# Optimization experiments

Measured on AMD Instinct MI355X. Metric: run time of the kernel, lower is better.

The kernel has to match this reference:

```python
import jax, jax.numpy as jnp
import numpy as np

D_MODEL = 1024
H = 16
D_K = D_MODEL // H
BAND = 100  # attention allowed where |i-j| < BAND


def setup_inputs() -> dict:
    key = jax.random.key(0)
    ks = jax.random.split(key, 9)
    B, S = 2, 2048
    s = 1.0 / np.sqrt(D_MODEL)
    return {
        "x": jax.random.normal(ks[0], (B, S, D_MODEL), jnp.float32),
        "Wq": jax.random.normal(ks[1], (D_MODEL, D_MODEL), jnp.float32) * s,
        "bq": jnp.zeros((D_MODEL,), jnp.float32),
        "Wk": jax.random.normal(ks[2], (D_MODEL, D_MODEL), jnp.float32) * s,
        "bk": jnp.zeros((D_MODEL,), jnp.float32),
        "Wv": jax.random.normal(ks[3], (D_MODEL, D_MODEL), jnp.float32) * s,
        "bv": jnp.zeros((D_MODEL,), jnp.float32),
        "Wo": jax.random.normal(ks[4], (D_MODEL, D_MODEL), jnp.float32) * s,
        "bo": jnp.zeros((D_MODEL,), jnp.float32),
    }


def _split_heads(t, B, S):
    # [B, S, D] -> [B, H, S, D_K]
    return t.reshape(B, S, H, D_K).transpose(0, 2, 1, 3)


def reference(x, Wq, bq, Wk, bk, Wv, bv, Wo, bo):
    B, S, _ = x.shape
    q = _split_heads(x @ Wq.T + bq, B, S)
    k = _split_heads(x @ Wk.T + bk, B, S)
    v = _split_heads(x @ Wv.T + bv, B, S)

    scores = jnp.einsum("bhqd,bhkd->bhqk", q, k) / jnp.sqrt(jnp.float32(D_K))
    i = jnp.arange(S)
    band = jnp.abs(i[:, None] - i[None, :]) < BAND  # [S, S] True inside band
    scores = jnp.where(band[None, None, :, :], scores, jnp.float32(-1e9))
    p_attn = jax.nn.softmax(scores, axis=-1)

    out = jnp.einsum("bhqk,bhkd->bhqd", p_attn, v)
    out = out.transpose(0, 2, 1, 3).reshape(B, S, D_MODEL)
    return out @ Wo.T + bo
```

## Files before the change

kernel.cpp:

```cpp
#include <hip/hip_runtime.h>
#include <hip/hip_bf16.h>


typedef __attribute__((ext_vector_type(8))) short short8;
typedef __attribute__((ext_vector_type(4))) float f32x4;

#define S_LEN 2048
#define NH 16
#define DK 64
#define BANDW 100

#define X_ELEMS   (2 * S_LEN * 1024)
#define W_ELEMS   (1024 * 1024)
#define QKV_ELEMS (2 * NH * S_LEN * DK)
#define AO_ELEMS  (2 * S_LEN * 1024)

__device__ __attribute__((aligned(256))) short g_X[X_ELEMS];
__device__ __attribute__((aligned(256))) short g_W[4 * W_ELEMS];
__device__ __attribute__((aligned(256))) short g_b[4 * 1024];
__device__ __attribute__((aligned(256))) short g_Q[QKV_ELEMS];
__device__ __attribute__((aligned(256))) short g_K[QKV_ELEMS];
__device__ __attribute__((aligned(256))) short g_V[QKV_ELEMS];
__device__ __attribute__((aligned(256))) short g_AO[AO_ELEMS];

__device__ __forceinline__ float bf2f(short u) {
    unsigned x = ((unsigned)(unsigned short)u) << 16;
    return __builtin_bit_cast(float, x);
}
__device__ __forceinline__ short f2bf(float f) {
    unsigned x = __builtin_bit_cast(unsigned, f);
    unsigned r = (x + 0x7fffu + ((x >> 16) & 1u)) >> 16;
    return (short)r;
}

#define GLOAD_LDS(gp, lp) \
    __builtin_amdgcn_global_load_lds( \
        (const __attribute__((address_space(1))) void*)(gp), \
        (__attribute__((address_space(3))) void*)(lp), 16, 0, 0)

#define XC   (X_ELEMS / 8)
#define WC   (W_ELEMS / 8)
#define BC   (1024 / 8)
#define TOTC (XC + 4 * WC + 4 * BC)

__global__ __launch_bounds__(256) void convert_all(
    const void* __restrict__ x,
    const void* __restrict__ w0, const void* __restrict__ b0,
    const void* __restrict__ w1, const void* __restrict__ b1,
    const void* __restrict__ w2, const void* __restrict__ b2,
    const void* __restrict__ w3, const void* __restrict__ b3)
{
    __shared__ int cnt[256];
    {
        const unsigned* xw = (const unsigned*)x;
        int local = 0;
        #pragma unroll
        for (int i = 0; i < 4; i++) {
            unsigned wv = xw[threadIdx.x * 4 + i];
            unsigned e = (wv >> 7) & 0xFF;
            if (e >= 100 && e <= 140) local++;
        }
        cnt[threadIdx.x] = local;
    }
    __syncthreads();
    for (int s = 128; s > 0; s >>= 1) {
        if (threadIdx.x < s) cnt[threadIdx.x] += cnt[threadIdx.x + s];
        __syncthreads();
    }
    const int is_bf16 = (cnt[0] > 512);

    long i = (long)blockIdx.x * 256 + threadIdx.x;
    if (i >= TOTC) return;

    const void* src; short* dst; long off;
    if (i < XC)                { src = x;  dst = g_X;              off = i; }
    else if ((i -= XC) < WC)   { src = w0; dst = g_W + 0L*W_ELEMS; off = i; }
    else if ((i -= WC) < WC)   { src = w1; dst = g_W + 1L*W_ELEMS; off = i; }
    else if ((i -= WC) < WC)   { src = w2; dst = g_W + 2L*W_ELEMS; off = i; }
    else if ((i -= WC) < WC)   { src = w3; dst = g_W + 3L*W_ELEMS; off = i; }
    else if ((i -= WC) < BC)   { src = b0; dst = g_b + 0*1024;     off = i; }
    else if ((i -= BC) < BC)   { src = b1; dst = g_b + 1*1024;     off = i; }
    else if ((i -= BC) < BC)   { src = b2; dst = g_b + 2*1024;     off = i; }
    else                       { src = b3; dst = g_b + 3*1024;     off = i - BC; }

    if (is_bf16) {
        ((short8*)dst)[off] = ((const short8*)src)[off];
    } else {
        const float* s = (const float*)src + off * 8;
        short8 o;
        #pragma unroll
        for (int e = 0; e < 8; e++) o[e] = f2bf(s[e]);
        ((short8*)dst)[off] = o;
    }
}


__global__ __launch_bounds__(256) void qkv_gemm()
{
    __shared__ __attribute__((aligned(16))) short As[128 * 32];
    __shared__ __attribute__((aligned(16))) short Bs[128 * 32];

    const int z = blockIdx.z;
    const short* __restrict__ X = g_X;
    const short* __restrict__ W = g_W + (long)z * W_ELEMS;
    const short* __restrict__ bias = g_b + z * 1024;
    short* __restrict__ Out = (z == 0) ? g_Q : ((z == 1) ? g_K : g_V);

    const int t = threadIdx.x;
    const int lane = t & 63;
    const int wid  = t >> 6;
    const int wm = wid & 1, wn = wid >> 1;
    const int l15 = lane & 15;
    const int q8  = (lane >> 4) * 8;
    const int mb = blockIdx.x * 128;
    const int nb = blockIdx.y * 128;

    const long ga0 = (long)(mb + (t >> 2)) * 1024 + (t & 3) * 8;
    const long ga1 = (long)(mb + 64 + (t >> 2)) * 1024 + (t & 3) * 8;
    const long gb0 = (long)(nb + (t >> 2)) * 1024 + (t & 3) * 8;
    const long gb1 = (long)(nb + 64 + (t >> 2)) * 1024 + (t & 3) * 8;
    short* lA0 = As + t * 8;
    short* lA1 = As + 2048 + t * 8;
    short* lB0 = Bs + t * 8;
    short* lB1 = Bs + 2048 + t * 8;

    f32x4 acc[4][4] = {};

    for (int k0 = 0; k0 < 1024; k0 += 32) {
        __syncthreads();
        GLOAD_LDS(X + ga0 + k0, lA0);
        GLOAD_LDS(X + ga1 + k0, lA1);
        GLOAD_LDS(W + gb0 + k0, lB0);
        GLOAD_LDS(W + gb1 + k0, lB1);
        __syncthreads();

        short8 a[4], b[4];
        #pragma unroll
        for (int mt = 0; mt < 4; mt++) a[mt] = *(const short8*)(As + (wm * 64 + mt * 16 + l15) * 32 + q8);
        #pragma unroll
        for (int nt = 0; nt < 4; nt++) b[nt] = *(const short8*)(Bs + (wn * 64 + nt * 16 + l15) * 32 + q8);
        #pragma unroll
        for (int mt = 0; mt < 4; mt++)
            #pragma unroll
            for (int nt = 0; nt < 4; nt++)
                acc[mt][nt] = __builtin_amdgcn_mfma_f32_16x16x32_bf16(a[mt], b[nt], acc[mt][nt], 0, 0, 0);
    }

    const int rg = (lane >> 4) * 4;
    #pragma unroll
    for (int nt = 0; nt < 4; nt++) {
        const int col = nb + wn * 64 + nt * 16 + l15;
        const float bv_ = bf2f(bias[col]);
        const int h = col >> 6, d = col & 63;
        #pragma unroll
        for (int mt = 0; mt < 4; mt++) {
            #pragma unroll
            for (int r = 0; r < 4; r++) {
                const int row = mb + wm * 64 + mt * 16 + rg + r;
                const int bI = row >> 11, s = row & 2047;
                Out[(((long)(bI * NH + h) * S_LEN) + s) * DK + d] = f2bf(acc[mt][nt][r] + bv_);
            }
        }
    }
}

__global__ __launch_bounds__(256) void o_gemm(float* __restrict__ Out)
{
    __shared__ __attribute__((aligned(16))) short As[128 * 32];
    __shared__ __attribute__((aligned(16))) short Bs[128 * 32];

    const short* __restrict__ A = g_AO;
    const short* __restrict__ W = g_W + 3L * W_ELEMS;

    const int t = threadIdx.x;
    const int lane = t & 63;
    const int wid  = t >> 6;
    const int wm = wid & 1, wn = wid >> 1;
    const int l15 = lane & 15;
    const int q8  = (lane >> 4) * 8;
    const int mb = blockIdx.x * 128;
    const int nb = blockIdx.y * 128;

    const long ga0 = (long)(mb + (t >> 2)) * 1024 + (t & 3) * 8;
    const long ga1 = (long)(mb + 64 + (t >> 2)) * 1024 + (t & 3) * 8;
    const long gb0 = (long)(nb + (t >> 2)) * 1024 + (t & 3) * 8;
    const long gb1 = (long)(nb + 64 + (t >> 2)) * 1024 + (t & 3) * 8;
    short* lA0 = As + t * 8;
    short* lA1 = As + 2048 + t * 8;
    short* lB0 = Bs + t * 8;
    short* lB1 = Bs + 2048 + t * 8;

    f32x4 acc[4][4] = {};

    for (int k0 = 0; k0 < 1024; k0 += 32) {
        __syncthreads();
        GLOAD_LDS(A + ga0 + k0, lA0);
        GLOAD_LDS(A + ga1 + k0, lA1);
        GLOAD_LDS(W + gb0 + k0, lB0);
        GLOAD_LDS(W + gb1 + k0, lB1);
        __syncthreads();

        short8 a[4], b[4];
        #pragma unroll
        for (int mt = 0; mt < 4; mt++) a[mt] = *(const short8*)(As + (wm * 64 + mt * 16 + l15) * 32 + q8);
        #pragma unroll
        for (int nt = 0; nt < 4; nt++) b[nt] = *(const short8*)(Bs + (wn * 64 + nt * 16 + l15) * 32 + q8);
        #pragma unroll
        for (int mt = 0; mt < 4; mt++)
            #pragma unroll
            for (int nt = 0; nt < 4; nt++)
                acc[mt][nt] = __builtin_amdgcn_mfma_f32_16x16x32_bf16(a[mt], b[nt], acc[mt][nt], 0, 0, 0);
    }

    const int rg = (lane >> 4) * 4;
    #pragma unroll
    for (int nt = 0; nt < 4; nt++) {
        const int col = nb + wn * 64 + nt * 16 + l15;
        const float bv_ = bf2f(g_b[3 * 1024 + col]);
        #pragma unroll
        for (int mt = 0; mt < 4; mt++) {
            #pragma unroll
            for (int r = 0; r < 4; r++) {
                const int row = mb + wm * 64 + mt * 16 + rg + r;
                Out[(long)row * 1024 + col] = acc[mt][nt][r] + bv_;
            }
        }
    }
}

__global__ __launch_bounds__(256) void attn_kernel()
{
    __shared__ __attribute__((aligned(16))) short Vt[64][72];
    __shared__ __attribute__((aligned(16))) short Pl[4][16][72];

    const int bid = blockIdx.x;
    const int qt = bid & 31;
    const int h  = (bid >> 5) & 15;
    const int b  = bid >> 9;
    const int qbase = qt * 64;

    const int lane = threadIdx.x & 63;
    const int w    = threadIdx.x >> 6;
    const int l15  = lane & 15;
    const int qg   = lane >> 4;
    const int q8   = qg * 8;

    const long hoff = (long)(b * NH + h) * S_LEN * DK;
    const short* __restrict__ Qh = g_Q + hoff;
    const short* __restrict__ Kh = g_K + hoff;
    const short* __restrict__ Vh = g_V + hoff;

    const short* qp = Qh + (long)(qbase + w * 16 + l15) * DK + q8;
    const short8 aq0 = *(const short8*)(qp);
    const short8 aq1 = *(const short8*)(qp + 32);

    f32x4 o[4] = {};
    float m_r[4], l_r[4];
    #pragma unroll
    for (int r = 0; r < 4; r++) { m_r[r] = -1e30f; l_r[r] = 0.f; }

    const int lo  = qbase - (BANDW - 1);
    const int kc0 = (lo < 0 ? 0 : lo) >> 6;
    int hi = qbase + 64 + (BANDW - 1);
    if (hi > S_LEN) hi = S_LEN;
    const int kc1 = (hi + 63) >> 6;

    for (int kc = kc0; kc < kc1; kc++) {
        const int kb = kc * 64;
        __syncthreads();
        {
            const int key = threadIdx.x >> 2;
            const int dq  = threadIdx.x & 3;
            const short8 v0 = *(const short8*)(Vh + (long)(kb + key) * DK + dq * 16);
            const short8 v1 = *(const short8*)(Vh + (long)(kb + key) * DK + dq * 16 + 8);
            #pragma unroll
            for (int e = 0; e < 8; e++) {
                Vt[dq * 16 + e][key]     = v0[e];
                Vt[dq * 16 + 8 + e][key] = v1[e];
            }
        }
        __syncthreads();

        f32x4 sc[4];
        #pragma unroll
        for (int nt = 0; nt < 4; nt++) {
            const short* kp = Kh + (long)(kb + nt * 16 + l15) * DK + q8;
            const short8 bk0 = *(const short8*)(kp);
            const short8 bk1 = *(const short8*)(kp + 32);
            f32x4 z = {};
            z = __builtin_amdgcn_mfma_f32_16x16x32_bf16(aq0, bk0, z, 0, 0, 0);
            z = __builtin_amdgcn_mfma_f32_16x16x32_bf16(aq1, bk1, z, 0, 0, 0);
            sc[nt] = z;
        }

        float pv[4][4];
        float mx[4] = {-1e30f, -1e30f, -1e30f, -1e30f};
        #pragma unroll
        for (int nt = 0; nt < 4; nt++) {
            const int kg = kb + nt * 16 + l15;
            #pragma unroll
            for (int r = 0; r < 4; r++) {
                const int qI = qbase + w * 16 + qg * 4 + r;
                int dlt = qI - kg; if (dlt < 0) dlt = -dlt;
                const float v = (dlt < BANDW) ? sc[nt][r] * 0.125f : -1e30f;
                pv[nt][r] = v;
                mx[r] = fmaxf(mx[r], v);
            }
        }
        #pragma unroll
        for (int mk = 1; mk < 16; mk <<= 1)
            #pragma unroll
            for (int r = 0; r < 4; r++) mx[r] = fmaxf(mx[r], __shfl_xor(mx[r], mk, 64));

        float alpha[4], lnew[4];
        #pragma unroll
        for (int r = 0; r < 4; r++) {
            const float mn = fmaxf(m_r[r], mx[r]);
            alpha[r] = __builtin_exp2f((m_r[r] - mn) * 1.44269504f);
            m_r[r] = mn;
            lnew[r] = 0.f;
        }
        #pragma unroll
        for (int nt = 0; nt < 4; nt++)
            #pragma unroll
            for (int r = 0; r < 4; r++) {
                const float p = (pv[nt][r] > -0.5e30f)
                    ? __builtin_exp2f((pv[nt][r] - m_r[r]) * 1.44269504f) : 0.f;
                pv[nt][r] = p;
                lnew[r] += p;
            }
        #pragma unroll
        for (int mk = 1; mk < 16; mk <<= 1)
            #pragma unroll
            for (int r = 0; r < 4; r++) lnew[r] += __shfl_xor(lnew[r], mk, 64);
        #pragma unroll
        for (int r = 0; r < 4; r++) l_r[r] = l_r[r] * alpha[r] + lnew[r];
        #pragma unroll
        for (int nt2 = 0; nt2 < 4; nt2++)
            #pragma unroll
            for (int r = 0; r < 4; r++) o[nt2][r] *= alpha[r];

        #pragma unroll
        for (int nt = 0; nt < 4; nt++)
            #pragma unroll
            for (int r = 0; r < 4; r++)
                Pl[w][qg * 4 + r][nt * 16 + l15] = f2bf(pv[nt][r]);
        asm volatile("s_waitcnt lgkmcnt(0)" ::: "memory");
        const short8 ap0 = *(const short8*)(&Pl[w][l15][q8]);
        const short8 ap1 = *(const short8*)(&Pl[w][l15][32 + q8]);

        #pragma unroll
        for (int nt2 = 0; nt2 < 4; nt2++) {
            const short8 bv0 = *(const short8*)(&Vt[nt2 * 16 + l15][q8]);
            const short8 bv1 = *(const short8*)(&Vt[nt2 * 16 + l15][32 + q8]);
            o[nt2] = __builtin_amdgcn_mfma_f32_16x16x32_bf16(ap0, bv0, o[nt2], 0, 0, 0);
            o[nt2] = __builtin_amdgcn_mfma_f32_16x16x32_bf16(ap1, bv1, o[nt2], 0, 0, 0);
        }
    }

    #pragma unroll
    for (int nt2 = 0; nt2 < 4; nt2++)
        #pragma unroll
        for (int r = 0; r < 4; r++) {
            const int qI = qbase + w * 16 + qg * 4 + r;
            const int d = nt2 * 16 + l15;
            g_AO[((long)b * S_LEN + qI) * 1024 + h * DK + d] = f2bf(o[nt2][r] / l_r[r]);
        }
}

extern "C" void kernel_launch(void* const* d_in, const int* in_sizes, int n_in,
                              void* d_out, int out_size, void* d_ws, size_t ws_size,
                              hipStream_t stream) {
    float* out = (float*)d_out;

    convert_all<<<(TOTC + 255) / 256, 256, 0, stream>>>(
        d_in[0], d_in[1], d_in[2], d_in[3], d_in[4], d_in[5], d_in[6], d_in[7], d_in[8]);
    qkv_gemm<<<dim3(32, 8, 3), 256, 0, stream>>>();
    attn_kernel<<<dim3(2 * NH * (S_LEN / 64)), 256, 0, stream>>>();
    o_gemm<<<dim3(32, 8), 256, 0, stream>>>(out);
}
```

Baseline: 180.7 us.

## Store V transposed from QKV GEMM and shrink O-GEMM N tile

The QKV GEMM epilogue now writes V in a [b,h,d,s] transposed layout using packed 4-element stores. The attention kernel then reads V fragments straight from global memory, dropping the per-chunk LDS transpose and its two barriers. Separately, the output projection GEMM uses 128x64 tiles with twice as many blocks, which raises block count and occupancy but reuses less data per block.

```diff
diff --git a/kernel.cpp b/kernel.cpp
--- a/kernel.cpp
+++ b/kernel.cpp
@@ -3,6 +3,7 @@
 
 
 typedef __attribute__((ext_vector_type(8))) short short8;
+typedef __attribute__((ext_vector_type(4))) short short4v;
 typedef __attribute__((ext_vector_type(4))) float f32x4;
 
 #define S_LEN 2048
@@ -94,7 +95,6 @@
     }
 }
 
-
 __global__ __launch_bounds__(256) void qkv_gemm()
 {
     __shared__ __attribute__((aligned(16))) short As[128 * 32];
@@ -104,7 +104,6 @@
     const short* __restrict__ X = g_X;
     const short* __restrict__ W = g_W + (long)z * W_ELEMS;
     const short* __restrict__ bias = g_b + z * 1024;
-    short* __restrict__ Out = (z == 0) ? g_Q : ((z == 1) ? g_K : g_V);
 
     const int t = threadIdx.x;
     const int lane = t & 63;
@@ -147,18 +146,37 @@
     }
 
     const int rg = (lane >> 4) * 4;
-    #pragma unroll
-    for (int nt = 0; nt < 4; nt++) {
-        const int col = nb + wn * 64 + nt * 16 + l15;
-        const float bv_ = bf2f(bias[col]);
-        const int h = col >> 6, d = col & 63;
-        #pragma unroll
-        for (int mt = 0; mt < 4; mt++) {
-            #pragma unroll
-            for (int r = 0; r < 4; r++) {
-                const int row = mb + wm * 64 + mt * 16 + rg + r;
-                const int bI = row >> 11, s = row & 2047;
-                Out[(((long)(bI * NH + h) * S_LEN) + s) * DK + d] = f2bf(acc[mt][nt][r] + bv_);
+    if (z == 2) {
+        #pragma unroll
+        for (int nt = 0; nt < 4; nt++) {
+            const int col = nb + wn * 64 + nt * 16 + l15;
+            const float bv_ = bf2f(bias[col]);
+            const int h = col >> 6, d = col & 63;
+            #pragma unroll
+            for (int mt = 0; mt < 4; mt++) {
+                const int row0 = mb + wm * 64 + mt * 16 + rg;
+                const int bI = row0 >> 11, s0 = row0 & 2047;
+                short4v pk;
+                #pragma unroll
+                for (int r = 0; r < 4; r++) pk[r] = f2bf(acc[mt][nt][r] + bv_);
+                *(short4v*)(g_V + (((long)(bI * NH + h) * DK) + d) * S_LEN + s0) = pk;
+            }
+        }
+    } else {
+        short* __restrict__ Out = (z == 0) ? g_Q : g_K;
+        #pragma unroll
+        for (int nt = 0; nt < 4; nt++) {
+            const int col = nb + wn * 64 + nt * 16 + l15;
+            const float bv_ = bf2f(bias[col]);
+            const int h = col >> 6, d = col & 63;
+            #pragma unroll
+            for (int mt = 0; mt < 4; mt++) {
+                #pragma unroll
+                for (int r = 0; r < 4; r++) {
+                    const int row = mb + wm * 64 + mt * 16 + rg + r;
+                    const int bI = row >> 11, s = row & 2047;
+                    Out[(((long)(bI * NH + h) * S_LEN) + s) * DK + d] = f2bf(acc[mt][nt][r] + bv_);
+                }
             }
         }
     }
@@ -167,7 +185,7 @@
 __global__ __launch_bounds__(256) void o_gemm(float* __restrict__ Out)
 {
     __shared__ __attribute__((aligned(16))) short As[128 * 32];
-    __shared__ __attribute__((aligned(16))) short Bs[128 * 32];
+    __shared__ __attribute__((aligned(16))) short Bs[64 * 32];
 
     const short* __restrict__ A = g_AO;
     const short* __restrict__ W = g_W + 3L * W_ELEMS;
@@ -179,43 +197,40 @@
     const int l15 = lane & 15;
     const int q8  = (lane >> 4) * 8;
     const int mb = blockIdx.x * 128;
-    const int nb = blockIdx.y * 128;
+    const int nb = blockIdx.y * 64;
 
     const long ga0 = (long)(mb + (t >> 2)) * 1024 + (t & 3) * 8;
     const long ga1 = (long)(mb + 64 + (t >> 2)) * 1024 + (t & 3) * 8;
     const long gb0 = (long)(nb + (t >> 2)) * 1024 + (t & 3) * 8;
-    const long gb1 = (long)(nb + 64 + (t >> 2)) * 1024 + (t & 3) * 8;
     short* lA0 = As + t * 8;
     short* lA1 = As + 2048 + t * 8;
     short* lB0 = Bs + t * 8;
-    short* lB1 = Bs + 2048 + t * 8;
-
-    f32x4 acc[4][4] = {};
+
+    f32x4 acc[4][2] = {};
 
     for (int k0 = 0; k0 < 1024; k0 += 32) {
         __syncthreads();
         GLOAD_LDS(A + ga0 + k0, lA0);
         GLOAD_LDS(A + ga1 + k0, lA1);
         GLOAD_LDS(W + gb0 + k0, lB0);
-        GLOAD_LDS(W + gb1 + k0, lB1);
-        __syncthreads();
-
-        short8 a[4], b[4];
+        __syncthreads();
+
+        short8 a[4], b[2];
         #pragma unroll
         for (int mt = 0; mt < 4; mt++) a[mt] = *(const short8*)(As + (wm * 64 + mt * 16 + l15) * 32 + q8);
         #pragma unroll
-        for (int nt = 0; nt < 4; nt++) b[nt] = *(const short8*)(Bs + (wn * 64 + nt * 16 + l15) * 32 + q8);
+        for (int nt = 0; nt < 2; nt++) b[nt] = *(const short8*)(Bs + (wn * 32 + nt * 16 + l15) * 32 + q8);
         #pragma unroll
         for (int mt = 0; mt < 4; mt++)
             #pragma unroll
-            for (int nt = 0; nt < 4; nt++)
+            for (int nt = 0; nt < 2; nt++)
                 acc[mt][nt] = __builtin_amdgcn_mfma_f32_16x16x32_bf16(a[mt], b[nt], acc[mt][nt], 0, 0, 0);
     }
 
     const int rg = (lane >> 4) * 4;
     #pragma unroll
-    for (int nt = 0; nt < 4; nt++) {
-        const int col = nb + wn * 64 + nt * 16 + l15;
+    for (int nt = 0; nt < 2; nt++) {
+        const int col = nb + wn * 32 + nt * 16 + l15;
         const float bv_ = bf2f(g_b[3 * 1024 + col]);
         #pragma unroll
         for (int mt = 0; mt < 4; mt++) {
@@ -230,7 +245,6 @@
 
 __global__ __launch_bounds__(256) void attn_kernel()
 {
-    __shared__ __attribute__((aligned(16))) short Vt[64][72];
     __shared__ __attribute__((aligned(16))) short Pl[4][16][72];
 
     const int bid = blockIdx.x;
@@ -248,7 +262,7 @@
     const long hoff = (long)(b * NH + h) * S_LEN * DK;
     const short* __restrict__ Qh = g_Q + hoff;
     const short* __restrict__ Kh = g_K + hoff;
-    const short* __restrict__ Vh = g_V + hoff;
+    const short* __restrict__ Vt = g_V + hoff;
 
     const short* qp = Qh + (long)(qbase + w * 16 + l15) * DK + q8;
     const short8 aq0 = *(const short8*)(qp);
@@ -267,19 +281,6 @@
 
     for (int kc = kc0; kc < kc1; kc++) {
         const int kb = kc * 64;
-        __syncthreads();
-        {
-            const int key = threadIdx.x >> 2;
-            const int dq  = threadIdx.x & 3;
-            const short8 v0 = *(const short8*)(Vh + (long)(kb + key) * DK + dq * 16);
-            const short8 v1 = *(const short8*)(Vh + (long)(kb + key) * DK + dq * 16 + 8);
-            #pragma unroll
-            for (int e = 0; e < 8; e++) {
-                Vt[dq * 16 + e][key]     = v0[e];
-                Vt[dq * 16 + 8 + e][key] = v1[e];
-            }
-        }
-        __syncthreads();
 
         f32x4 sc[4];
         #pragma unroll
@@ -351,8 +352,9 @@
 
         #pragma unroll
         for (int nt2 = 0; nt2 < 4; nt2++) {
-            const short8 bv0 = *(const short8*)(&Vt[nt2 * 16 + l15][q8]);
-            const short8 bv1 = *(const short8*)(&Vt[nt2 * 16 + l15][32 + q8]);
+            const short* vp = Vt + (long)(nt2 * 16 + l15) * S_LEN + kb;
+            const short8 bv0 = *(const short8*)(vp + q8);
+            const short8 bv1 = *(const short8*)(vp + 32 + q8);
             o[nt2] = __builtin_amdgcn_mfma_f32_16x16x32_bf16(ap0, bv0, o[nt2], 0, 0, 0);
             o[nt2] = __builtin_amdgcn_mfma_f32_16x16x32_bf16(ap1, bv1, o[nt2], 0, 0, 0);
         }
@@ -377,5 +379,5 @@
         d_in[0], d_in[1], d_in[2], d_in[3], d_in[4], d_in[5], d_in[6], d_in[7], d_in[8]);
     qkv_gemm<<<dim3(32, 8, 3), 256, 0, stream>>>();
     attn_kernel<<<dim3(2 * NH * (S_LEN / 64)), 256, 0, stream>>>();
-    o_gemm<<<dim3(32, 8), 256, 0, stream>>>(out);
-}
+    o_gemm<<<dim3(32, 16), 256, 0, stream>>>(out);
+}
```

Result: slower. 198.1 us (+9.7%).
